# Performance work log

Measured on AMD Instinct MI355X. Metric: run time of the kernel, lower is better.

The kernel has to match this reference:

```python
import jax, jax.numpy as jnp
import numpy as np

B = 2          # batch
L = 2048       # seq len
D_MODEL = 1024
D_INNER = 2 * D_MODEL   # expand = 2
D_STATE = 16
D_CONV = 4
DT_RANK = D_MODEL // 16  # 64


def setup_inputs() -> dict:
    key = jax.random.key(0)
    kx, kf, kb = jax.random.split(key, 3)
    d = {"x": jax.random.normal(kx, (B, L, D_MODEL), jnp.float32)}
    for pre, k in (("f_", kf), ("b_", kb)):
        kk = jax.random.split(k, 6)
        d[pre + "in_proj_w"] = jax.random.normal(kk[0], (2 * D_INNER, D_MODEL), jnp.float32) * 0.02
        d[pre + "conv_w"] = jax.random.normal(kk[1], (D_INNER, 1, D_CONV), jnp.float32) * 0.2
        d[pre + "conv_b"] = jnp.zeros((D_INNER,), jnp.float32)
        d[pre + "x_proj_w"] = jax.random.normal(kk[2], (DT_RANK + 2 * D_STATE, D_INNER), jnp.float32) * 0.02
        d[pre + "dt_proj_w"] = jax.random.normal(kk[3], (D_INNER, DT_RANK), jnp.float32) * 0.02
        # dt bias init so softplus(bias) ~ dt in [exp(-4), exp(-2)] range (mamba-style)
        d[pre + "dt_proj_b"] = jax.random.uniform(kk[4], (D_INNER,), jnp.float32, minval=-4.0, maxval=-2.0)
        # S4D-real init: A = -[1..d_state]
        d[pre + "A_log"] = jnp.log(jnp.broadcast_to(jnp.arange(1, D_STATE + 1, dtype=jnp.float32), (D_INNER, D_STATE)))
        d[pre + "D"] = jnp.ones((D_INNER,), jnp.float32)
        d[pre + "out_proj_w"] = jax.random.normal(kk[5], (D_MODEL, D_INNER), jnp.float32) * 0.02
    return d


def _silu(x):
    return x * jax.nn.sigmoid(x)


def _selective_scan(u, dt, A, Bm, Cm, Dp):
    # u, dt: [B, L, d_inner]; Bm, Cm: [B, L, d_state]; A: [d_inner, d_state]; Dp: [d_inner]
    def step(h, inp):
        u_t, dt_t, B_t, C_t = inp                       # [B,d], [B,d], [B,n], [B,n]
        dA = jnp.exp(dt_t[..., None] * A)               # [B, d, n]  (ZOH discretization)
        dBu = dt_t[..., None] * B_t[:, None, :] * u_t[..., None]
        h = dA * h + dBu                                # [B, d, n]
        y = jnp.einsum('bdn,bn->bd', h, C_t)            # [B, d]
        return h, y

    h0 = jnp.zeros((u.shape[0], A.shape[0], A.shape[1]), u.dtype)
    xs = (jnp.swapaxes(u, 0, 1), jnp.swapaxes(dt, 0, 1),
          jnp.swapaxes(Bm, 0, 1), jnp.swapaxes(Cm, 0, 1))
    _, ys = jax.lax.scan(step, h0, xs)                  # ys: [L, B, d_inner]
    return jnp.swapaxes(ys, 0, 1) + u * Dp              # skip connection D*u


def _mamba(x, in_proj_w, conv_w, conv_b, x_proj_w, dt_proj_w, dt_proj_b, A_log, Dp, out_proj_w):
    # x: [B, L, d_model]
    xz = x @ in_proj_w.T                                # [B, L, 2*d_inner]
    xi, z = jnp.split(xz, 2, axis=-1)
    # depthwise causal conv1d, kernel D_CONV, output truncated to L (left pad)
    xc = jax.lax.conv_general_dilated(
        jnp.swapaxes(xi, 1, 2), conv_w, (1,), [(D_CONV - 1, 0)],
        dimension_numbers=('NCH', 'OIH', 'NCH'), feature_group_count=D_INNER)
    xi = _silu(jnp.swapaxes(xc, 1, 2) + conv_b)         # [B, L, d_inner]
    x_dbl = xi @ x_proj_w.T                             # [B, L, dt_rank + 2*d_state]
    dt, Bm, Cm = jnp.split(x_dbl, [DT_RANK, DT_RANK + D_STATE], axis=-1)
    dt = jax.nn.softplus(dt @ dt_proj_w.T + dt_proj_b)  # [B, L, d_inner]
    A = -jnp.exp(A_log)                                 # [d_inner, d_state]
    y = _selective_scan(xi, dt, A, Bm, Cm, Dp)
    y = y * _silu(z)                                    # gated
    return y @ out_proj_w.T                             # [B, L, d_model]


def reference(x,
              f_in_proj_w, f_conv_w, f_conv_b, f_x_proj_w, f_dt_proj_w, f_dt_proj_b, f_A_log, f_D, f_out_proj_w,
              b_in_proj_w, b_conv_w, b_conv_b, b_x_proj_w, b_dt_proj_w, b_dt_proj_b, b_A_log, b_D, b_out_proj_w):
    h_fwd = _mamba(x, f_in_proj_w, f_conv_w, f_conv_b, f_x_proj_w,
                   f_dt_proj_w, f_dt_proj_b, f_A_log, f_D, f_out_proj_w)
    h_bwd = _mamba(jnp.flip(x, axis=1), b_in_proj_w, b_conv_w, b_conv_b, b_x_proj_w,
                   b_dt_proj_w, b_dt_proj_b, b_A_log, b_D, b_out_proj_w)
    h_bwd = jnp.flip(h_bwd, axis=1)
    return jnp.concatenate([h_fwd, h_bwd], axis=-1)     # [B, L, 2*d_model]
```

## Files before the change

kernel.cpp:

```cpp
#include <hip/hip_runtime.h>

#define BB 2
#define LL 2048
#define DM 1024
#define DI 2048
#define NTOK (BB*LL)
#define NC 64
#define CL (LL/NC)
#define NCH (BB*DI)

typedef __bf16 bf16x8 __attribute__((ext_vector_type(8)));
typedef float f32x4 __attribute__((ext_vector_type(4)));
typedef int i32x4 __attribute__((ext_vector_type(4)));

#define LOG2E 1.44269504088896340736f

__device__ __forceinline__ float siluf(float x){ return x / (1.f + __expf(-x)); }
__device__ __forceinline__ float softplusf(float x){
  if (x > 20.f) return x;
  return log1pf(__expf(x));
}
__device__ __forceinline__ unsigned short f2bf(float f){
  unsigned int u = __builtin_bit_cast(unsigned int, f);
  u += 0x7fffu + ((u >> 16) & 1u);
  return (unsigned short)(u >> 16);
}
__device__ __forceinline__ float bf2f(unsigned short u){
  return __builtin_bit_cast(float, (unsigned int)u << 16);
}
template<typename CT>
__device__ __forceinline__ void st_ct(CT* p, float v){
  if constexpr (sizeof(CT)==2) *p = (CT)f2bf(v); else *p = (CT)v;
}

__device__ __forceinline__ void gl_lds16(const unsigned short* g, unsigned short* l){
  __builtin_amdgcn_global_load_lds(
      (const __attribute__((address_space(1))) void*)g,
      (__attribute__((address_space(3))) void*)l, 16, 0, 0);
}

#define SEG0 4096
#define SEG1 8192
#define SEG2 512
#define SEG3 256
#define SEG4 4096
#define CAST_BLOCKS (SEG0+SEG1+SEG2+SEG3+SEG4)

__device__ __forceinline__ void cast4(const float* src, unsigned short* dst){
  float4 v = *reinterpret_cast<const float4*>(src);
  ushort4 o; o.x=f2bf(v.x); o.y=f2bf(v.y); o.z=f2bf(v.z); o.w=f2bf(v.w);
  *reinterpret_cast<ushort4*>(dst) = o;
}

__global__ __launch_bounds__(256) void k_cast_all(
    const float* __restrict__ x,
    const float* __restrict__ ipw0, const float* __restrict__ ipw1,
    const float* __restrict__ xpw0, const float* __restrict__ xpw1,
    const float* __restrict__ dtw0, const float* __restrict__ dtw1,
    const float* __restrict__ opw0, const float* __restrict__ opw1,
    unsigned short* __restrict__ x_bf, unsigned short* __restrict__ w_bf,
    unsigned short* __restrict__ wpad, unsigned short* __restrict__ dtw_bf,
    unsigned short* __restrict__ outw){
  int bid = blockIdx.x;
  int ti = threadIdx.x*4;
  if (bid < SEG0){
    int i = bid*1024 + ti;
    cast4(x + i, x_bf + i);
  } else if (bid < SEG0+SEG1){
    int i = (bid-SEG0)*1024 + ti;
    const int n = (2*DI)*DM;
    const float* src = (i < n) ? ipw0 : ipw1;
    int off = (i < n) ? i : i - n;
    cast4(src + off, w_bf + i);
  } else if (bid < SEG0+SEG1+SEG2){
    int i = (bid-SEG0-SEG1)*1024 + ti;
    const int ntotal = 128*DI, nreal = 96*DI;
    int dir = i / ntotal;
    int r = i - dir*ntotal;
    if (r < nreal){
      cast4((dir ? xpw1 : xpw0) + r, wpad + i);
    } else {
      ushort4 z{0,0,0,0};
      *reinterpret_cast<ushort4*>(wpad + i) = z;
    }
  } else if (bid < SEG0+SEG1+SEG2+SEG3){
    int i = (bid-SEG0-SEG1-SEG2)*1024 + ti;
    const int n = DI*64;
    const float* src = (i < n) ? dtw0 : dtw1;
    int off = (i < n) ? i : i - n;
    cast4(src + off, dtw_bf + i);
  } else {
    int i = (bid-SEG0-SEG1-SEG2-SEG3)*1024 + ti;
    const int n = DM*DI;
    const float* src = (i < n) ? opw0 : opw1;
    int off = (i < n) ? i : i - n;
    cast4(src + off, outw + i);
  }
}

template<int NT>
__global__ __launch_bounds__(512) void k_gemm256(
    const unsigned short* __restrict__ A, int lda,
    const unsigned short* __restrict__ Bw, int ldb, long long bz,
    unsigned short* __restrict__ C, unsigned short* __restrict__ C2, int nsplit,
    int ldc, long long cz){
  __shared__ unsigned short L[65536];
  const int dir = blockIdx.z;
  Bw += (size_t)dir*bz;
  const int m0 = blockIdx.y*256;
  const int bn0 = blockIdx.x*256;
  unsigned short* Cout; int n0;
  if (bn0 < nsplit){ Cout = C; n0 = bn0; } else { Cout = C2; n0 = bn0 - nsplit; }
  Cout += (size_t)dir*cz;

  const int tid = threadIdx.x;
  const int w = tid >> 6, lane = tid & 63;
  const int rT = tid >> 2;
  const int sG = (tid & 3) ^ ((tid >> 3) & 3);
  const unsigned short* srcA = A  + (size_t)(m0  + rT)*lda + sG*8;
  const unsigned short* srcB = Bw + (size_t)(bn0 + rT)*ldb + sG*8;
  unsigned short* const lw = &L[w*512];
  const int wmb = (w>>2)*128, wnb = (w&3)*64;
  const int fr = lane & 15;
  const int sk = ((lane>>4) ^ ((fr>>1)&3))*8;

  f32x4 acc[8][4] = {};

  auto STAGE = [&](int kt, int kk, int c){
    const unsigned short* a_ = srcA + kt*64 + kk*32;
    const unsigned short* b_ = srcB + kt*64 + kk*32;
    unsigned short* l_ = lw + c*32768 + kk*16384;
    gl_lds16(a_,                   l_);
    gl_lds16(a_ + (size_t)128*lda, l_ + 4096);
    gl_lds16(b_,                   l_ + 8192);
    gl_lds16(b_ + (size_t)128*ldb, l_ + 12288);
  };

  auto HALF = [&](int c, int kk, bool stage, int kt){
    if (stage) STAGE(kt, kk, c^1);
    const unsigned short* base = &L[c*32768 + kk*16384];
    bf16x8 a[8];
#pragma unroll
    for (int i=0;i<8;i++)
      a[i] = *reinterpret_cast<const bf16x8*>(&base[(wmb + i*16 + fr)*32 + sk]);
    bf16x8 b0 = *reinterpret_cast<const bf16x8*>(&base[8192 + (wnb +  0 + fr)*32 + sk]);
    bf16x8 b1 = *reinterpret_cast<const bf16x8*>(&base[8192 + (wnb + 16 + fr)*32 + sk]);
    __builtin_amdgcn_s_setprio(1);
#pragma unroll
    for (int i=0;i<8;i++){
      acc[i][0] = __builtin_amdgcn_mfma_f32_16x16x32_bf16(a[i], b0, acc[i][0], 0,0,0);
      acc[i][1] = __builtin_amdgcn_mfma_f32_16x16x32_bf16(a[i], b1, acc[i][1], 0,0,0);
    }
    __builtin_amdgcn_s_setprio(0);
    bf16x8 b2 = *reinterpret_cast<const bf16x8*>(&base[8192 + (wnb + 32 + fr)*32 + sk]);
    bf16x8 b3 = *reinterpret_cast<const bf16x8*>(&base[8192 + (wnb + 48 + fr)*32 + sk]);
    __builtin_amdgcn_s_setprio(1);
#pragma unroll
    for (int i=0;i<8;i++){
      acc[i][2] = __builtin_amdgcn_mfma_f32_16x16x32_bf16(a[i], b2, acc[i][2], 0,0,0);
      acc[i][3] = __builtin_amdgcn_mfma_f32_16x16x32_bf16(a[i], b3, acc[i][3], 0,0,0);
    }
    __builtin_amdgcn_s_setprio(0);
  };

  STAGE(0, 0, 0);
  STAGE(0, 1, 0);
#pragma unroll 2
  for (int t = 0; t < NT-1; ++t){
    const int c = t & 1;
    asm volatile("s_waitcnt vmcnt(4)" ::: "memory");
    asm volatile("s_barrier" ::: "memory");
    HALF(c, 0, true, t+1);
    asm volatile("s_waitcnt vmcnt(4)" ::: "memory");
    asm volatile("s_barrier" ::: "memory");
    HALF(c, 1, true, t+1);
  }
  {
    const int c = (NT-1) & 1;
    asm volatile("s_waitcnt vmcnt(4)" ::: "memory");
    asm volatile("s_barrier" ::: "memory");
    HALF(c, 0, false, 0);
    asm volatile("s_waitcnt vmcnt(0)" ::: "memory");
    asm volatile("s_barrier" ::: "memory");
    HALF(c, 1, false, 0);
  }

  const int er = (lane>>4)*4;
#pragma unroll
  for (int i=0;i<8;i++)
#pragma unroll
    for (int j=0;j<4;j++){
      int row = m0 + wmb + i*16 + er;
      int col = n0 + wnb + j*16 + fr;
      unsigned short* cp = Cout + (size_t)row*ldc + col;
#pragma unroll
      for (int r=0;r<4;r++) cp[(size_t)r*ldc] = f2bf(acc[i][j][r]);
    }
}

template<int EPI, int KSPLIT, typename CT>
__global__ __launch_bounds__(256) void k_gemm_bt(
    const unsigned short* __restrict__ A, int lda, long long az,
    const unsigned short* __restrict__ Bw, int ldb, long long bz,
    CT* __restrict__ C, CT* __restrict__ C2, int nsplit,
    int ldc, long long cz, int coffz,
    int K, int coff,
    const float* __restrict__ bias0, const float* __restrict__ bias1){
  __shared__ unsigned short As[3*128*32];
  __shared__ unsigned short Bs[3*128*32];
  const int z = blockIdx.z;
  const int dirz = z / KSPLIT, kc = z - dirz*KSPLIT;
  A  += (size_t)dirz*az + (size_t)kc*K;
  Bw += (size_t)dirz*bz + (size_t)kc*K;
  const int bn0 = blockIdx.x*128;
  int n0 = bn0;
  if (bn0 >= nsplit){ C = C2; n0 = bn0 - nsplit; }
  C  += (size_t)z*cz;
  const int co = coff + dirz*coffz;
  const float* bias = dirz ? bias1 : bias0;

  const int t = threadIdx.x;
  const int m0 = blockIdx.y*128;
  const int lane = t & 63, w = t >> 6;
  const int wm = (w>>1)*64, wn = (w&1)*64;

  const int gr = lane >> 2;
  const int gslot = (lane & 3) ^ ((lane >> 3) & 3);
  const unsigned short* gA = A  + (size_t)(m0  + 32*w + gr)*lda + gslot*8;
  const unsigned short* gB = Bw + (size_t)(bn0 + 32*w + gr)*ldb + gslot*8;
  unsigned short* lA = &As[(32*w)*32];
  unsigned short* lB = &Bs[(32*w)*32];

  f32x4 acc[4][4] = {};
  const int fr = lane & 15;
  const int rslot = ((lane>>4) ^ ((lane>>1)&3))*8;

  const int NTk = K >> 5;
  auto STG = [&](int kt, int c){
    gl_lds16(gA + kt*32, lA + c*4096);
    gl_lds16(gA + (size_t)16*lda + kt*32, lA + c*4096 + 16*32);
    gl_lds16(gB + kt*32, lB + c*4096);
    gl_lds16(gB + (size_t)16*ldb + kt*32, lB + c*4096 + 16*32);
  };
  STG(0, 0);
  if (NTk > 1) STG(1, 1);
  int c = 0, cs = 2;
  for (int kt = 0; kt < NTk; ++kt){
    if (kt < NTk-1){ asm volatile("s_waitcnt vmcnt(4)" ::: "memory"); }
    else           { asm volatile("s_waitcnt vmcnt(0)" ::: "memory"); }
    asm volatile("s_barrier" ::: "memory");
    if (kt+2 < NTk) STG(kt+2, cs);
    bf16x8 af[4], bfr[4];
#pragma unroll
    for (int i=0;i<4;i++){
      af[i]  = *reinterpret_cast<const bf16x8*>(&As[c*4096 + (wm + i*16 + fr)*32 + rslot]);
      bfr[i] = *reinterpret_cast<const bf16x8*>(&Bs[c*4096 + (wn + i*16 + fr)*32 + rslot]);
    }
#pragma unroll
    for (int i=0;i<4;i++)
#pragma unroll
      for (int j=0;j<4;j++)
        acc[i][j] = __builtin_amdgcn_mfma_f32_16x16x32_bf16(af[i], bfr[j], acc[i][j], 0,0,0);
    c = (c==2) ? 0 : c+1;
    cs = (cs==2) ? 0 : cs+1;
  }
  const int er = (lane>>4)*4;
#pragma unroll
  for (int i=0;i<4;i++)
#pragma unroll
    for (int j=0;j<4;j++){
      int row = m0 + wm + i*16 + er;
      int bcol = n0 + wn + j*16 + fr;
      CT* cp = C + (size_t)row*ldc + co + bcol;
      if (EPI == 1){
        float bv = bias[bcol];
#pragma unroll
        for (int r=0;r<4;r++) st_ct(&cp[(size_t)r*ldc], softplusf(acc[i][j][r] + bv));
      } else {
#pragma unroll
        for (int r=0;r<4;r++) st_ct(&cp[(size_t)r*ldc], acc[i][j][r]);
      }
    }
}

__global__ __launch_bounds__(256) void k_conv_silu(const unsigned short* __restrict__ xpre,
    const float* __restrict__ cw0, const float* __restrict__ cw1,
    const float* __restrict__ cb0, const float* __restrict__ cb1,
    unsigned short* __restrict__ xi_bf){
  const int dir = blockIdx.z;
  const int d0 = threadIdx.x*8;
  const int tok0 = blockIdx.x*4;
  const int b = tok0 >> 11;
  const int t0 = tok0 & (LL-1);
  const float* cw = dir ? cw1 : cw0;
  const float* cb = dir ? cb1 : cb0;
  const unsigned short* xpd = xpre + (size_t)dir*NTOK*DI;
  unsigned short* outp = xi_bf + (size_t)dir*NTOK*DI;

  float wv[4][8];
#pragma unroll
  for (int c=0;c<8;c++){
    float4 w = *reinterpret_cast<const float4*>(cw + (size_t)(d0+c)*4);
    wv[0][c]=w.x; wv[1][c]=w.y; wv[2][c]=w.z; wv[3][c]=w.w;
  }
  float bv[8];
  {
    float4 b0 = *reinterpret_cast<const float4*>(cb + d0);
    float4 b1 = *reinterpret_cast<const float4*>(cb + d0 + 4);
    bv[0]=b0.x; bv[1]=b0.y; bv[2]=b0.z; bv[3]=b0.w;
    bv[4]=b1.x; bv[5]=b1.y; bv[6]=b1.z; bv[7]=b1.w;
  }
  const int rbase = t0 + (dir ? 0 : -3);
  float rows[7][8];
#pragma unroll
  for (int i=0;i<7;i++){
    int r = rbase + i;
    if (r >= 0 && r < LL){
      union { i32x4 v; unsigned short u[8]; } x;
      x.v = *reinterpret_cast<const i32x4*>(xpd + ((size_t)b*LL + r)*DI + d0);
#pragma unroll
      for (int c=0;c<8;c++) rows[i][c] = bf2f(x.u[c]);
    } else {
#pragma unroll
      for (int c=0;c<8;c++) rows[i][c] = 0.f;
    }
  }
#pragma unroll
  for (int j=0;j<4;j++){
    union { i32x4 v; unsigned short u[8]; } o;
#pragma unroll
    for (int c=0;c<8;c++){
      float acc = bv[c];
#pragma unroll
      for (int m=0;m<4;m++){
        float w = dir ? wv[3-m][c] : wv[m][c];
        acc += w * rows[j+m][c];
      }
      o.u[c] = f2bf(siluf(acc));
    }
    *reinterpret_cast<i32x4*>(outp + ((size_t)(tok0+j))*DI + d0) = o.v;
  }
}

__global__ __launch_bounds__(256) void k_xred(const float* __restrict__ part,
    float* __restrict__ xdbl, unsigned short* __restrict__ xdbl_bf){
  int idx = blockIdx.x*256 + threadIdx.x;
  if (idx >= 2*NTOK*96) return;
  int dir = idx / (NTOK*96);
  int rem = idx - dir*(NTOK*96);
  int tok = rem / 96, j = rem - tok*96;
  const float* pd = part + (size_t)dir*4*NTOK*128;
  const size_t czs = (size_t)NTOK*128;
  size_t o = (size_t)tok*128 + j;
  float v = pd[o] + pd[czs + o] + pd[2*czs + o] + pd[3*czs + o];
  xdbl[(size_t)dir*NTOK*96 + (size_t)tok*96 + j] = v;
  if (j < 64) xdbl_bf[(size_t)dir*NTOK*64 + (size_t)tok*64 + j] = f2bf(v);
}

__device__ __forceinline__ void powtree(float q, float* dA){
  dA[0]=q;
  dA[1]=dA[0]*dA[0];
  dA[2]=dA[1]*dA[0];
  dA[3]=dA[1]*dA[1];
  dA[4]=dA[3]*dA[0];
  dA[5]=dA[3]*dA[1];
  dA[6]=dA[3]*dA[2];
  dA[7]=dA[3]*dA[3];
#pragma unroll
  for (int n=8;n<16;n++) dA[n]=dA[7]*dA[n-8];
}
__device__ __forceinline__ bool chk_struct(const float* Alog2){
  bool ok = true;
  float a0 = Alog2[0];
#pragma unroll
  for (int n=1;n<16;n++){
    float e = a0*(float)(n+1);
    ok = ok && (fabsf(Alog2[n]-e) <= 1e-5f*fabsf(e) + 1e-12f);
  }
  return ok;
}

__global__ __launch_bounds__(256) void k_scan_p1(const unsigned short* __restrict__ u,
    const unsigned short* __restrict__ dt, const float* __restrict__ xdbl,
    const float* __restrict__ A_log0, const float* __restrict__ A_log1,
    float* __restrict__ hloc, float* __restrict__ dtsum){
  __shared__ float Bs[CL*16];
  const int dir = blockIdx.z;
  u    += (size_t)dir*NTOK*DI;
  dt   += (size_t)dir*NTOK*DI;
  xdbl += (size_t)dir*NTOK*96;
  const float* A_log = dir ? A_log1 : A_log0;
  const int tid = threadIdx.x;
  const int ch = blockIdx.x*256 + tid;
  const int c = blockIdx.y;
  const int b = (blockIdx.x*256) >> 11;
  const int d = ch & (DI-1);
  for (int i = tid; i < CL*16; i += 256){
    int s = i >> 4, j = i & 15;
    int sg = c*CL + s;
    int tt = dir ? (LL-1-sg) : sg;
    Bs[i] = xdbl[((size_t)b*LL + tt)*96 + 64 + j];
  }
  float Alog2[16];
  {
    const float4* ap = reinterpret_cast<const float4*>(A_log + (size_t)d*16);
#pragma unroll
    for (int q=0;q<4;q++){
      float4 v = ap[q];
      Alog2[q*4+0] = -__expf(v.x)*LOG2E;
      Alog2[q*4+1] = -__expf(v.y)*LOG2E;
      Alog2[q*4+2] = -__expf(v.z)*LOG2E;
      Alog2[q*4+3] = -__expf(v.w)*LOG2E;
    }
  }
  const bool structured = chk_struct(Alog2);
  __syncthreads();
  float h[16];
#pragma unroll
  for (int n=0;n<16;n++) h[n]=0.f;
  float dts = 0.f;
  int tok0 = b*LL + (dir ? (LL-1-c*CL) : c*CL);
  const unsigned short* up = u + (size_t)tok0*DI + d;
  const unsigned short* dtp = dt + (size_t)tok0*DI + d;
  const ptrdiff_t stp = dir ? -(ptrdiff_t)DI : (ptrdiff_t)DI;
  if (structured){
    const float a0 = Alog2[0];
#pragma unroll 2
    for (int s=0; s<CL; s++){
      float uv  = bf2f(*up); up += stp;
      float dtv = bf2f(*dtp); dtp += stp;
      float dtu = dtv*uv;
      dts += dtv;
      const f32x4* br = reinterpret_cast<const f32x4*>(&Bs[s*16]);
      f32x4 B0=br[0], B1=br[1], B2=br[2], B3=br[3];
      float dA[16];
      powtree(__builtin_amdgcn_exp2f(dtv*a0), dA);
#pragma unroll
      for (int n=0;n<16;n++){
        float Bv = (n<4)?B0[n&3] : (n<8)?B1[n&3] : (n<12)?B2[n&3] : B3[n&3];
        h[n] = dA[n]*h[n] + dtu*Bv;
      }
    }
  } else {
#pragma unroll 2
    for (int s=0; s<CL; s++){
      float uv  = bf2f(*up); up += stp;
      float dtv = bf2f(*dtp); dtp += stp;
      float dtu = dtv*uv;
      dts += dtv;
      const f32x4* br = reinterpret_cast<const f32x4*>(&Bs[s*16]);
      f32x4 B0=br[0], B1=br[1], B2=br[2], B3=br[3];
#pragma unroll
      for (int n=0;n<16;n++){
        float dA = __builtin_amdgcn_exp2f(dtv*Alog2[n]);
        float Bv = (n<4)?B0[n&3] : (n<8)?B1[n&3] : (n<12)?B2[n&3] : B3[n&3];
        h[n] = dA*h[n] + dtu*Bv;
      }
    }
  }
  float* hp = hloc + (((size_t)(dir*NC + c)*NCH + ch))*16;
#pragma unroll
  for (int q=0;q<4;q++)
    *reinterpret_cast<f32x4*>(hp + q*4) = f32x4{h[q*4],h[q*4+1],h[q*4+2],h[q*4+3]};
  dtsum[(size_t)(dir*NC + c)*NCH + ch] = dts;
}

__global__ __launch_bounds__(256) void k_scan_comb(float* __restrict__ hloc,
    const float* __restrict__ dtsum,
    const float* __restrict__ A_log0, const float* __restrict__ A_log1){
  int i = blockIdx.x*256 + threadIdx.x;
  int dir = i / (NCH*16);
  int j = i - dir*(NCH*16);
  int ch = j >> 4, n = j & 15;
  int d = ch & (DI-1);
  const float* A_log = dir ? A_log1 : A_log0;
  float Alog2 = -__expf(A_log[(size_t)d*16 + n])*LOG2E;
  float hs = 0.f;
#pragma unroll 4
  for (int c=0; c<NC; c++){
    size_t base = (size_t)(dir*NC + c)*NCH + ch;
    float pa = __builtin_amdgcn_exp2f(dtsum[base]*Alog2);
    size_t idx = base*16 + n;
    float h = hloc[idx];
    hloc[idx] = hs;
    hs = pa*hs + h;
  }
}

__global__ __launch_bounds__(256) void k_scan_p2(unsigned short* __restrict__ uy,
    const unsigned short* __restrict__ dt, const float* __restrict__ xdbl,
    const unsigned short* __restrict__ zbuf,
    const float* __restrict__ A_log0, const float* __restrict__ A_log1,
    const float* __restrict__ Dp0, const float* __restrict__ Dp1,
    const float* __restrict__ hstart){
  __shared__ float BCs[CL*32];
  const int dir = blockIdx.z;
  uy   += (size_t)dir*NTOK*DI;
  dt   += (size_t)dir*NTOK*DI;
  zbuf += (size_t)dir*NTOK*DI;
  xdbl += (size_t)dir*NTOK*96;
  const float* A_log = dir ? A_log1 : A_log0;
  const float* Dp = dir ? Dp1 : Dp0;
  const int tid = threadIdx.x;
  const int ch = blockIdx.x*256 + tid;
  const int c = blockIdx.y;
  const int b = (blockIdx.x*256) >> 11;
  const int d = ch & (DI-1);
  for (int i = tid; i < CL*32; i += 256){
    int s = i >> 5, j = i & 31;
    int sg = c*CL + s;
    int tt = dir ? (LL-1-sg) : sg;
    BCs[i] = xdbl[((size_t)b*LL + tt)*96 + 64 + j];
  }
  float Alog2[16];
  {
    const float4* ap = reinterpret_cast<const float4*>(A_log + (size_t)d*16);
#pragma unroll
    for (int q=0;q<4;q++){
      float4 v = ap[q];
      Alog2[q*4+0] = -__expf(v.x)*LOG2E;
      Alog2[q*4+1] = -__expf(v.y)*LOG2E;
      Alog2[q*4+2] = -__expf(v.z)*LOG2E;
      Alog2[q*4+3] = -__expf(v.w)*LOG2E;
    }
  }
  const bool structured = chk_struct(Alog2);
  float h[16];
  {
    const float* hp = hstart + (((size_t)(dir*NC + c)*NCH + ch))*16;
#pragma unroll
    for (int q=0;q<4;q++){
      f32x4 v = *reinterpret_cast<const f32x4*>(hp + q*4);
      h[q*4]=v[0]; h[q*4+1]=v[1]; h[q*4+2]=v[2]; h[q*4+3]=v[3];
    }
  }
  const float Dval = Dp[d];
  __syncthreads();
  int tok0 = b*LL + (dir ? (LL-1-c*CL) : c*CL);
  unsigned short* up = uy + (size_t)tok0*DI + d;
  const unsigned short* zp = zbuf + (size_t)tok0*DI + d;
  const unsigned short* dtp = dt + (size_t)tok0*DI + d;
  const ptrdiff_t stp = dir ? -(ptrdiff_t)DI : (ptrdiff_t)DI;
  if (structured){
    const float a0 = Alog2[0];
#pragma unroll 2
    for (int s=0; s<CL; s++){
      float uv  = bf2f(*up);
      float zv  = bf2f(*zp); zp += stp;
      float dtv = bf2f(*dtp); dtp += stp;
      float dtu = dtv*uv;
      float y = Dval*uv;
      const f32x4* br = reinterpret_cast<const f32x4*>(&BCs[s*32]);
      f32x4 B0=br[0], B1=br[1], B2=br[2], B3=br[3];
      f32x4 C0=br[4], C1=br[5], C2=br[6], C3=br[7];
      float dA[16];
      powtree(__builtin_amdgcn_exp2f(dtv*a0), dA);
#pragma unroll
      for (int n=0;n<16;n++){
        float Bv = (n<4)?B0[n&3] : (n<8)?B1[n&3] : (n<12)?B2[n&3] : B3[n&3];
        float Cv = (n<4)?C0[n&3] : (n<8)?C1[n&3] : (n<12)?C2[n&3] : C3[n&3];
        h[n] = dA[n]*h[n] + dtu*Bv;
        y += h[n]*Cv;
      }
      *up = f2bf(y * siluf(zv)); up += stp;
    }
  } else {
#pragma unroll 2
    for (int s=0; s<CL; s++){
      float uv  = bf2f(*up);
      float zv  = bf2f(*zp); zp += stp;
      float dtv = bf2f(*dtp); dtp += stp;
      float dtu = dtv*uv;
      float y = Dval*uv;
      const f32x4* br = reinterpret_cast<const f32x4*>(&BCs[s*32]);
      f32x4 B0=br[0], B1=br[1], B2=br[2], B3=br[3];
      f32x4 C0=br[4], C1=br[5], C2=br[6], C3=br[7];
#pragma unroll
      for (int n=0;n<16;n++){
        float dA = __builtin_amdgcn_exp2f(dtv*Alog2[n]);
        float Bv = (n<4)?B0[n&3] : (n<8)?B1[n&3] : (n<12)?B2[n&3] : B3[n&3];
        float Cv = (n<4)?C0[n&3] : (n<8)?C1[n&3] : (n<12)?C2[n&3] : C3[n&3];
        h[n] = dA*h[n] + dtu*Bv;
        y += h[n]*Cv;
      }
      *up = f2bf(y * siluf(zv)); up += stp;
    }
  }
}

extern "C" void kernel_launch(void* const* d_in, const int* in_sizes, int n_in,
                              void* d_out, int out_size, void* d_ws, size_t ws_size,
                              hipStream_t stream){
  (void)in_sizes; (void)n_in; (void)out_size; (void)ws_size;
  const float* x = (const float*)d_in[0];
  const float* ipw[2], *cw[2], *cb[2], *xpw[2], *dtw_[2], *dtb[2], *Alog[2], *Dp[2], *opw[2];
  for (int dir=0; dir<2; dir++){
    ipw[dir]  = (const float*)d_in[1 + dir*9 + 0];
    cw[dir]   = (const float*)d_in[1 + dir*9 + 1];
    cb[dir]   = (const float*)d_in[1 + dir*9 + 2];
    xpw[dir]  = (const float*)d_in[1 + dir*9 + 3];
    dtw_[dir] = (const float*)d_in[1 + dir*9 + 4];
    dtb[dir]  = (const float*)d_in[1 + dir*9 + 5];
    Alog[dir] = (const float*)d_in[1 + dir*9 + 6];
    Dp[dir]   = (const float*)d_in[1 + dir*9 + 7];
    opw[dir]  = (const float*)d_in[1 + dir*9 + 8];
  }
  char* p = (char*)d_ws;
  auto alloc = [&](size_t bytes)->void*{ void* r=(void*)p; p += (bytes+255)&~(size_t)255; return r; };
  unsigned short* x_bf   = (unsigned short*)alloc((size_t)NTOK*DM*2);
  unsigned short* w_bf   = (unsigned short*)alloc((size_t)2*(2*DI)*DM*2);
  float* part            = (float*)w_bf;
  unsigned short* xpre   = (unsigned short*)alloc((size_t)2*NTOK*DI*2);
  unsigned short* zbuf   = (unsigned short*)alloc((size_t)2*NTOK*DI*2);
  unsigned short* xi_bf  = (unsigned short*)alloc((size_t)2*NTOK*DI*2);
  float* xdbl            = (float*)alloc((size_t)2*NTOK*96*4);
  unsigned short* xdbl_bf= (unsigned short*)alloc((size_t)2*NTOK*64*2);
  unsigned short* dt_bf  = (unsigned short*)alloc((size_t)2*NTOK*DI*2);
  unsigned short* wpad   = (unsigned short*)alloc((size_t)2*128*DI*2);
  unsigned short* dtw_bf = (unsigned short*)alloc((size_t)2*DI*64*2);
  unsigned short* outw   = (unsigned short*)alloc((size_t)2*DM*DI*2);
  float* hloc  = (float*)d_ws;
  float* dtsum = (float*)((char*)d_ws + (size_t)32*1024*1024);

  k_cast_all<<<CAST_BLOCKS, 256, 0, stream>>>(
      x, ipw[0], ipw[1], xpw[0], xpw[1], dtw_[0], dtw_[1], opw[0], opw[1],
      x_bf, w_bf, wpad, dtw_bf, outw);

  k_gemm256<16><<<dim3(16,16,2), 512, 0, stream>>>(
      x_bf, DM, w_bf, DM, (long long)(2*DI)*DM,
      xpre, zbuf, DI, DI, (long long)NTOK*DI);
  k_conv_silu<<<dim3(NTOK/4,1,2), 256, 0, stream>>>(xpre, cw[0], cw[1], cb[0], cb[1], xi_bf);
  k_gemm_bt<0,4,float><<<dim3(1,32,8), 256, 0, stream>>>(
      xi_bf, DI, (long long)NTOK*DI, wpad, DI, (long long)128*DI,
      part, part, 1<<30, 128, (long long)NTOK*128, 0, 512, 0, nullptr, nullptr);
  k_xred<<<(2*NTOK*96+255)/256, 256, 0, stream>>>(part, xdbl, xdbl_bf);
  k_gemm_bt<1,1,unsigned short><<<dim3(16,32,2), 256, 0, stream>>>(
      xdbl_bf, 64, (long long)NTOK*64, dtw_bf, 64, (long long)DI*64,
      dt_bf, dt_bf, 1<<30, DI, (long long)NTOK*DI, 0, 64, 0, dtb[0], dtb[1]);
  k_scan_p1<<<dim3(NCH/256, NC, 2), 256, 0, stream>>>(xi_bf, dt_bf, xdbl,
      Alog[0], Alog[1], hloc, dtsum);
  k_scan_comb<<<2*NCH*16/256, 256, 0, stream>>>(hloc, dtsum, Alog[0], Alog[1]);
  k_scan_p2<<<dim3(NCH/256, NC, 2), 256, 0, stream>>>(xi_bf, dt_bf, xdbl, zbuf,
      Alog[0], Alog[1], Dp[0], Dp[1], hloc);
  k_gemm_bt<0,1,float><<<dim3(8,32,2), 256, 0, stream>>>(
      xi_bf, DI, (long long)NTOK*DI, outw, DI, (long long)DM*DI,
      (float*)d_out, (float*)d_out, 1<<30, 2*DM, 0, DM, DI, 0, nullptr, nullptr);
}
```

Baseline: 364.3 us.

## Swizzle 256-tile GEMM block order and single-buffer the 128-tile GEMM

The 256x256 GEMM now remaps its flat block index so that groups of eight consecutive blocks are spread across tiles. This is meant to better match the round-robin XCD dispatch and improve L2 reuse. The mapping assumes a 16x16x2 grid. The 128x128 GEMM drops its three-stage async global-to-LDS pipeline in favour of a single LDS buffer guarded by two barriers per k-step. That cuts LDS use, which may raise occupancy, but it loses the overlap of loads with MFMA work.

```diff
diff --git a/kernel.cpp b/kernel.cpp
--- a/kernel.cpp
+++ b/kernel.cpp
@@ -105,10 +105,12 @@
     unsigned short* __restrict__ C, unsigned short* __restrict__ C2, int nsplit,
     int ldc, long long cz){
   __shared__ unsigned short L[65536];
-  const int dir = blockIdx.z;
+  const int flat = blockIdx.x + (blockIdx.y<<4) + (blockIdx.z<<8);
+  const int swz = ((flat & 7) << 6) + (flat >> 3);
+  const int bx = swz & 15, by = (swz >> 4) & 15, dir = swz >> 8;
   Bw += (size_t)dir*bz;
-  const int m0 = blockIdx.y*256;
-  const int bn0 = blockIdx.x*256;
+  const int m0 = by*256;
+  const int bn0 = bx*256;
   unsigned short* Cout; int n0;
   if (bn0 < nsplit){ Cout = C; n0 = bn0; } else { Cout = C2; n0 = bn0 - nsplit; }
   Cout += (size_t)dir*cz;
@@ -206,8 +208,8 @@
     int ldc, long long cz, int coffz,
     int K, int coff,
     const float* __restrict__ bias0, const float* __restrict__ bias1){
-  __shared__ unsigned short As[3*128*32];
-  __shared__ unsigned short Bs[3*128*32];
+  __shared__ unsigned short As[128*32];
+  __shared__ unsigned short Bs[128*32];
   const int z = blockIdx.z;
   const int dirz = z / KSPLIT, kc = z - dirz*KSPLIT;
   A  += (size_t)dirz*az + (size_t)kc*K;
@@ -235,34 +237,24 @@
   const int fr = lane & 15;
   const int rslot = ((lane>>4) ^ ((lane>>1)&3))*8;
 
-  const int NTk = K >> 5;
-  auto STG = [&](int kt, int c){
-    gl_lds16(gA + kt*32, lA + c*4096);
-    gl_lds16(gA + (size_t)16*lda + kt*32, lA + c*4096 + 16*32);
-    gl_lds16(gB + kt*32, lB + c*4096);
-    gl_lds16(gB + (size_t)16*ldb + kt*32, lB + c*4096 + 16*32);
-  };
-  STG(0, 0);
-  if (NTk > 1) STG(1, 1);
-  int c = 0, cs = 2;
-  for (int kt = 0; kt < NTk; ++kt){
-    if (kt < NTk-1){ asm volatile("s_waitcnt vmcnt(4)" ::: "memory"); }
-    else           { asm volatile("s_waitcnt vmcnt(0)" ::: "memory"); }
-    asm volatile("s_barrier" ::: "memory");
-    if (kt+2 < NTk) STG(kt+2, cs);
+  for (int k0=0; k0<K; k0+=32){
+    __syncthreads();
+    gl_lds16(gA + k0, lA);
+    gl_lds16(gA + (size_t)16*lda + k0, lA + 16*32);
+    gl_lds16(gB + k0, lB);
+    gl_lds16(gB + (size_t)16*ldb + k0, lB + 16*32);
+    __syncthreads();
     bf16x8 af[4], bfr[4];
 #pragma unroll
     for (int i=0;i<4;i++){
-      af[i]  = *reinterpret_cast<const bf16x8*>(&As[c*4096 + (wm + i*16 + fr)*32 + rslot]);
-      bfr[i] = *reinterpret_cast<const bf16x8*>(&Bs[c*4096 + (wn + i*16 + fr)*32 + rslot]);
+      af[i]  = *reinterpret_cast<const bf16x8*>(&As[(wm + i*16 + fr)*32 + rslot]);
+      bfr[i] = *reinterpret_cast<const bf16x8*>(&Bs[(wn + i*16 + fr)*32 + rslot]);
     }
 #pragma unroll
     for (int i=0;i<4;i++)
 #pragma unroll
       for (int j=0;j<4;j++)
         acc[i][j] = __builtin_amdgcn_mfma_f32_16x16x32_bf16(af[i], bfr[j], acc[i][j], 0,0,0);
-    c = (c==2) ? 0 : c+1;
-    cs = (cs==2) ? 0 : cs+1;
   }
   const int er = (lane>>4)*4;
 #pragma unroll
```

Result: slower. 378.0 us (+3.8%).
